# Kernel tuning notes

Measured on AMD Instinct MI355X. Metric: run time of the kernel, lower is better.

## Reference

```python
import jax, jax.numpy as jnp
import numpy as np
import math

DIM = 1024      # dim == dim_attn (required by value-reshape)
HEAD = 16
KV = 128        # K_v routing slots
HD = DIM // HEAD
N = 50000       # number of nodes


def setup_inputs() -> dict:
    key = jax.random.key(0)
    ks = jax.random.split(key, 8)
    s = lambda fan_in: 1.0 / np.sqrt(fan_in)
    return {
        "x": jax.random.normal(ks[0], (N, DIM), jnp.float32),
        "node_index": jax.random.normal(ks[1], (N, 4), jnp.float32),
        # nn.Linear(dim, dim_attn)
        "Wq": jax.random.normal(ks[2], (DIM, DIM), jnp.float32) * s(DIM),
        "bq": jnp.zeros((DIM,), jnp.float32),
        # nn.Parameter key (K_v, head, head_dim), torch.randn init
        "key_p": jax.random.normal(ks[3], (KV, HEAD, HD), jnp.float32),
        # nn.Linear(dim, dim)
        "Wv": jax.random.normal(ks[4], (DIM, DIM), jnp.float32) * s(DIM),
        "bv": jnp.zeros((DIM,), jnp.float32),
        # gate params, shape (head, 1)
        "alpha": jnp.full((HEAD, 1), math.log(9.0), jnp.float32),
        "beta": jnp.full((HEAD, 1), math.log(0.01), jnp.float32),
        # nn.Linear(4, head*K_v)
        "Wb": jax.random.normal(ks[5], (HEAD * KV, 4), jnp.float32) * s(4),
        "bb": jnp.zeros((HEAD * KV,), jnp.float32),
    }


def _mh_sinkhorn(A, num_iters=3, eps=0.05):
    # A: (N, H, K). Faithful to the per-head torch sinkhorn (Q transposed to
    # (K, N)): row sums are over the node axis, col sums over the slot axis.
    n = A.shape[0]
    k = A.shape[2]
    Q = jnp.exp(A / eps)
    Q = Q / jnp.sum(Q, axis=(0, 2), keepdims=True)          # total-sum norm per head
    for _ in range(num_iters):
        Q = Q / jnp.sum(Q, axis=0, keepdims=True) / k       # rows of Q.T (per slot)
        Q = Q / jnp.sum(Q, axis=2, keepdims=True) / n       # cols of Q.T (per node)
    return Q * n


def reference(x, node_index, Wq, bq, key_p, Wv, bv, alpha, beta, Wb, bb):
    n = x.shape[0]
    q = (x @ Wq.T + bq).reshape(n, HEAD, HD)
    attn = jnp.einsum('nhd,rhd->nhr', q, key_p) / np.float32(np.sqrt(HD))
    bias = (node_index @ Wb.T + bb).reshape(n, HEAD, KV)
    attn = attn + bias                                       # (n, H, K_v)
    xv = (x @ Wv.T + bv).reshape(n, HEAD, HD)
    v = jnp.einsum('nhr,nhd->rhd', jax.nn.sigmoid(attn), xv)  # (K_v, H, D)
    cons = _mh_sinkhorn(jax.nn.softmax(attn, axis=-1))
    v = jnp.einsum('nhr,rhd->nhd', cons, v)
    out = jax.nn.sigmoid(alpha) * xv + jax.nn.sigmoid(beta) * v  # (H,1) broadcasts
    return out.reshape(n, DIM)
```

## Files before the change

### kernel.cpp

```cpp
#include <hip/hip_runtime.h>

#define N_NODES 50000
#define MPAD    50176
#define DIM     1024
#define HEAD    16
#define KV      128
#define HD      64
#define NGRP    98

typedef unsigned short ushort_t;
typedef short short8 __attribute__((ext_vector_type(8)));
typedef float f32x4 __attribute__((ext_vector_type(4)));

__device__ inline unsigned short f2bf(float f){
  union { float f; unsigned u; } v; v.f = f;
  unsigned u = v.u;
  unsigned r = (u + 0x7FFFu + ((u >> 16) & 1u)) >> 16;
  return (unsigned short)r;
}
__device__ inline float bf2f(unsigned u16){
  union { unsigned u; float f; } v; v.u = (u16 & 0xFFFFu) << 16; return v.f;
}

__device__ inline void gload_lds16(const void* g, void* l){
  __builtin_amdgcn_global_load_lds(
      (const __attribute__((address_space(1))) void*)g,
      (__attribute__((address_space(3))) void*)l, 16, 0, 0);
}

__device__ inline short8 frag64(const ushort_t* lds, int row, int kk, int lane){
  int c  = kk*4 + (lane >> 4);
  int cc = c ^ (row & 7);
  return *(const short8*)(lds + row*64 + cc*8);
}
__device__ inline short8 frag128(const ushort_t* lds, int row, int kk, int lane){
  int c  = kk*4 + (lane >> 4);
  int cc = c ^ (row & 7);
  return *(const short8*)(lds + row*128 + cc*8);
}

__global__ void k_zero(float* p, int n){
  int i = blockIdx.x*256 + threadIdx.x;
  if (i < n) p[i] = 0.f;
}

__global__ void k_prep_x(const float* __restrict__ x, ushort_t* __restrict__ x_bf){
  int idx = blockIdx.x*256 + threadIdx.x;
  int row = idx >> 7, c = idx & 127;
  const float4* s = (const float4*)(x + (size_t)row*1024 + c*8);
  float4 f0 = s[0], f1 = s[1];
  short8 v;
  v[0]=(short)f2bf(f0.x); v[1]=(short)f2bf(f0.y); v[2]=(short)f2bf(f0.z); v[3]=(short)f2bf(f0.w);
  v[4]=(short)f2bf(f1.x); v[5]=(short)f2bf(f1.y); v[6]=(short)f2bf(f1.z); v[7]=(short)f2bf(f1.w);
  int sc = (c & ~7) | ((c ^ row) & 7);
  *(short8*)(x_bf + (size_t)row*1024 + sc*8) = v;
}

__global__ void k_prep_w(const float* __restrict__ Wq, const float* __restrict__ Wv,
                         ushort_t* __restrict__ w_bf){
  int idx = blockIdx.x*256 + threadIdx.x;
  int j = idx >> 10, k = idx & 1023;
  float v = (j < 1024) ? Wq[idx] : Wv[(size_t)(j-1024)*1024 + k];
  int d = k & 63;
  int scol = (k & ~63) | ((((d>>3) ^ (j & 7)) & 7) << 3) | (d & 7);
  w_bf[(size_t)j*1024 + scol] = f2bf(v);
}

__global__ void k_prep_key(const float* __restrict__ key_p, ushort_t* __restrict__ key_bf){
  int idx = blockIdx.x*256 + threadIdx.x;
  int h = idx >> 13, rem = idx & 8191;
  int r = rem >> 6, d = rem & 63;
  float v = key_p[(size_t)(r*HEAD + h)*HD + d];
  int pos = ((((d>>3) ^ (r & 7)) & 7) << 3) | (d & 7);
  key_bf[(size_t)h*8192 + r*64 + pos] = f2bf(v);
}

__global__ void k_vreduce(const float* __restrict__ vp, float* __restrict__ vout){
  int i = blockIdx.x*256 + threadIdx.x;
  float s = 0.f;
  for (int gg = 0; gg < NGRP; ++gg) s += vp[(size_t)gg*131072 + i];
  vout[i] = s;
}

__global__ __launch_bounds__(512) void k_gemm(const ushort_t* __restrict__ x_bf,
    const ushort_t* __restrict__ w_bf, const float* __restrict__ bq,
    const float* __restrict__ bv, ushort_t* __restrict__ q_bf, float* xv_out){
  extern __shared__ char gsm[];
  ushort_t* As = (ushort_t*)gsm;
  ushort_t* Bs = (ushort_t*)(gsm + 65536);
  const int tid = threadIdx.x, lane = tid & 63;
  const int wid = tid >> 6, wr = wid >> 2, wc = wid & 3;
  int b = blockIdx.x;
  int wg = (b & 7)*196 + (b >> 3);
  const int bm0 = (wg >> 3) * 256, bn0 = (wg & 7) * 256;

  f32x4 acc[8][4];
  #pragma unroll
  for (int m=0;m<8;m++)
    #pragma unroll
    for (int n=0;n<4;n++) acc[m][n] = (f32x4){0.f,0.f,0.f,0.f};

  const ushort_t* asrc = x_bf + (size_t)bm0*1024;
  const ushort_t* bsrc = w_bf + (size_t)bn0*1024;

#define STAGE(kt, bi)                                                    \
  { _Pragma("unroll")                                                    \
    for (int it=0; it<4; ++it){                                          \
      int chunk = it*512 + tid;                                          \
      int r = chunk >> 3, c = chunk & 7;                                 \
      gload_lds16(asrc + (size_t)r*1024 + (kt)*64 + c*8,                 \
                  As + (bi)*16384 + chunk*8);                            \
    }                                                                    \
    _Pragma("unroll")                                                    \
    for (int it=0; it<4; ++it){                                          \
      int chunk = it*512 + tid;                                          \
      int r = chunk >> 3, c = chunk & 7;                                 \
      gload_lds16(bsrc + (size_t)r*1024 + (kt)*64 + c*8,                 \
                  Bs + (bi)*16384 + chunk*8);                            \
    }                                                                    \
  }

  STAGE(0, 0);
  STAGE(1, 1);

  for (int kt = 0; kt < 16; ++kt){
    const int cur = kt & 1;
    if (kt == 15) { asm volatile("s_waitcnt vmcnt(0)" ::: "memory"); }
    else          { asm volatile("s_waitcnt vmcnt(8)" ::: "memory"); }
    __builtin_amdgcn_s_barrier();

    const ushort_t* ab  = As + cur*16384;
    const ushort_t* bb_ = Bs + cur*16384;
    #pragma unroll
    for (int kk=0;kk<2;kk++){
      short8 bfr[4];
      #pragma unroll
      for (int n=0;n<4;n++) bfr[n] = frag64(bb_, wc*64 + n*16 + (lane&15), kk, lane);
      #pragma unroll
      for (int m=0;m<8;m++){
        short8 af = frag64(ab, wr*128 + m*16 + (lane&15), kk, lane);
        #pragma unroll
        for (int n=0;n<4;n++)
          acc[m][n] = __builtin_amdgcn_mfma_f32_16x16x32_bf16(af, bfr[n], acc[m][n], 0,0,0);
      }
    }
    __builtin_amdgcn_s_barrier();
    if (kt + 2 < 16) STAGE(kt+2, cur);
  }
#undef STAGE

  __syncthreads();

  const bool isq = bn0 < 1024;
  float biasv[4];
  #pragma unroll
  for (int n=0;n<4;n++){
    int col = bn0 + wc*64 + n*16 + (lane & 15);
    biasv[n] = isq ? bq[col] : bv[col - 1024];
  }

  if (isq){
    ushort_t* img = (ushort_t*)gsm;
    #pragma unroll
    for (int n=0;n<4;n++){
      int lcol = wc*64 + n*16 + (lane & 15);
      int d = lcol & 63;
      #pragma unroll
      for (int m=0;m<8;m++){
        #pragma unroll
        for (int j=0;j<4;j++){
          int lrow = wr*128 + m*16 + (lane>>4)*4 + j;
          int sc = (lcol & ~63) | ((((d>>3) ^ (lrow & 7)) & 7) << 3) | (d & 7);
          img[lrow*256 + sc] = f2bf(acc[m][n][j] + biasv[n]);
        }
      }
    }
    __syncthreads();
    #pragma unroll
    for (int it=0; it<16; ++it){
      int r  = it*16 + (tid >> 5);
      int ch = tid & 31;
      short8 v = *(const short8*)(img + r*256 + ch*8);
      *(short8*)(q_bf + (size_t)(bm0 + r)*1024 + bn0 + ch*8) = v;
    }
  } else {
    #pragma unroll
    for (int n=0;n<4;n++){
      int col = bn0 + wc*64 + n*16 + (lane & 15);
      #pragma unroll
      for (int m=0;m<8;m++){
        #pragma unroll
        for (int j=0;j<4;j++){
          int row = bm0 + wr*128 + m*16 + (lane>>4)*4 + j;
          if (row < N_NODES)
            xv_out[(size_t)row*1024 + (col - 1024)] = acc[m][n][j] + biasv[n];
        }
      }
    }
  }
}

__global__ __launch_bounds__(256) void k_s1(const ushort_t* __restrict__ q_bf,
    const ushort_t* __restrict__ key_bf, const float* __restrict__ ni,
    const float* __restrict__ Wb, const float* __restrict__ bb,
    const float* __restrict__ cs_in, float* __restrict__ cs_out){
  __shared__ float col_acc[4][128];
  const int tid = threadIdx.x, lane = tid & 63, wid = tid >> 6;
  const int h   = blockIdx.x & 15;
  const int blk = blockIdx.x >> 4;
  const int gw  = blk*4 + wid;
  const int cl  = lane & 15, rg = lane >> 4;

  float wbv[8][4], bbr[8], wv[8];
  #pragma unroll
  for (int n=0;n<8;n++){
    int r = h*128 + n*16 + cl;
    float4 w4 = *(const float4*)(Wb + (size_t)r*4);
    wbv[n][0]=w4.x; wbv[n][1]=w4.y; wbv[n][2]=w4.z; wbv[n][3]=w4.w;
    bbr[n] = bb[r];
    wv[n]  = 1.f/(128.f*cs_in[r]);
  }
  short8 kf[8][2];
  #pragma unroll
  for (int n=0;n<8;n++)
    #pragma unroll
    for (int kk=0;kk<2;kk++){
      int c = (kk*4+rg) ^ (cl & 7);
      kf[n][kk] = *(const short8*)(key_bf + (size_t)h*8192 + (n*16+cl)*64 + c*8);
    }

  float cs_acc[8];
  #pragma unroll
  for (int n=0;n<8;n++) cs_acc[n] = 0.f;

  const int g0 = gw*8;
  short8 qc[2], qn[2];
  { int row = g0*16 + cl;
    #pragma unroll
    for (int kk=0;kk<2;kk++){
      int c = (kk*4+rg) ^ (row & 7);
      qc[kk] = *(const short8*)(q_bf + (size_t)row*1024 + h*64 + c*8);
    } }

  for (int u = 0; u < 8; ++u){
    const int i0 = (g0+u)*16;
    if (u+1 < 8){
      int row = i0 + 16 + cl;
      #pragma unroll
      for (int kk=0;kk<2;kk++){
        int c = (kk*4+rg) ^ (row & 7);
        qn[kk] = *(const short8*)(q_bf + (size_t)row*1024 + h*64 + c*8);
      }
    }
    float4 ni4[4];
    #pragma unroll
    for (int j=0;j<4;j++){
      int row = i0 + rg*4 + j;
      if (row < N_NODES) ni4[j] = *(const float4*)(ni + (size_t)row*4);
      else { ni4[j].x=0.f; ni4[j].y=0.f; ni4[j].z=0.f; ni4[j].w=0.f; }
    }
    f32x4 acc[8];
    #pragma unroll
    for (int n=0;n<8;n++) acc[n] = (f32x4){0.f,0.f,0.f,0.f};
    #pragma unroll
    for (int n=0;n<8;n++){
      acc[n] = __builtin_amdgcn_mfma_f32_16x16x32_bf16(qc[0], kf[n][0], acc[n], 0,0,0);
      acc[n] = __builtin_amdgcn_mfma_f32_16x16x32_bf16(qc[1], kf[n][1], acc[n], 0,0,0);
    }
    float a[8][4];
    #pragma unroll
    for (int n=0;n<8;n++)
      #pragma unroll
      for (int j=0;j<4;j++)
        a[n][j] = acc[n][j]*0.125f
                + wbv[n][0]*ni4[j].x + wbv[n][1]*ni4[j].y
                + wbv[n][2]*ni4[j].z + wbv[n][3]*ni4[j].w + bbr[n];

    float mj[4], sj[4];
    #pragma unroll
    for (int j=0;j<4;j++){
      float m0 = a[0][j];
      #pragma unroll
      for (int n=1;n<8;n++) m0 = fmaxf(m0, a[n][j]);
      m0 = fmaxf(m0, __shfl_xor(m0,1));
      m0 = fmaxf(m0, __shfl_xor(m0,2));
      m0 = fmaxf(m0, __shfl_xor(m0,4));
      m0 = fmaxf(m0, __shfl_xor(m0,8));
      mj[j] = m0;
    }
    #pragma unroll
    for (int j=0;j<4;j++){
      float s = 0.f;
      #pragma unroll
      for (int n=0;n<8;n++){ float e = __expf(a[n][j]-mj[j]); a[n][j]=e; s+=e; }
      s += __shfl_xor(s,1); s += __shfl_xor(s,2);
      s += __shfl_xor(s,4); s += __shfl_xor(s,8);
      sj[j] = s;
    }
    #pragma unroll
    for (int j=0;j<4;j++){
      float inv = 20.f/sj[j];
      #pragma unroll
      for (int n=0;n<8;n++) a[n][j] = __expf(a[n][j]*inv);
    }
    float uj[4];
    #pragma unroll
    for (int j=0;j<4;j++){
      float s = 0.f;
      #pragma unroll
      for (int n=0;n<8;n++) s += a[n][j]*wv[n];
      s += __shfl_xor(s,1); s += __shfl_xor(s,2);
      s += __shfl_xor(s,4); s += __shfl_xor(s,8);
      int row = i0 + rg*4 + j;
      uj[j] = (row < N_NODES) ? 1.f/(50000.f*s) : 0.f;
    }
    #pragma unroll
    for (int n=0;n<8;n++)
      cs_acc[n] += a[n][0]*uj[0] + a[n][1]*uj[1] + a[n][2]*uj[2] + a[n][3]*uj[3];

    qc[0] = qn[0]; qc[1] = qn[1];
  }

  #pragma unroll
  for (int n=0;n<8;n++){
    float v = cs_acc[n];
    v += __shfl_xor(v,16); v += __shfl_xor(v,32);
    cs_acc[n] = v;
  }
  if (rg == 0){
    #pragma unroll
    for (int n=0;n<8;n++) col_acc[wid][n*16+cl] = cs_acc[n];
  }
  __syncthreads();
  if (tid < 128)
    atomicAdd(&cs_out[h*128+tid],
      col_acc[0][tid]+col_acc[1][tid]+col_acc[2][tid]+col_acc[3][tid]);
}

__global__ __launch_bounds__(256) void k_s2(const ushort_t* __restrict__ q_bf,
    const ushort_t* __restrict__ key_bf, const float* __restrict__ ni,
    const float* __restrict__ Wb, const float* __restrict__ bb,
    const float* __restrict__ cs_in, const float* __restrict__ v_fin,
    float* xv_out, const float* __restrict__ alpha, const float* __restrict__ beta){
  __shared__ ushort_t key_lds[128*64];
  __shared__ ushort_t vT[64*128];
  __shared__ ushort_t consW[4][16*128];
  const int tid = threadIdx.x, lane = tid & 63, wid = tid >> 6;
  const int h   = blockIdx.x & 15;
  const int blk = blockIdx.x >> 4;
  const int gw  = blk*4 + wid;
  const int cl  = lane & 15, rg = lane >> 4;

  #pragma unroll
  for (int it = 0; it < 4; ++it){
    int chunk = it*256 + tid;
    gload_lds16(key_bf + (size_t)h*8192 + chunk*8, key_lds + chunk*8);
  }
  { int r = tid >> 1, dh = (tid & 1)*32;
    #pragma unroll
    for (int i=0;i<32;i++){
      int d = dh + i;
      vT[d*128 + ((r>>3) ^ (d&7))*8 + (r&7)] = f2bf(v_fin[((size_t)r*16 + h)*64 + d]);
    } }

  float wbv[8][4], bbr[8], wv[8];
  #pragma unroll
  for (int n=0;n<8;n++){
    int r = h*128 + n*16 + cl;
    float4 w4 = *(const float4*)(Wb + (size_t)r*4);
    wbv[n][0]=w4.x; wbv[n][1]=w4.y; wbv[n][2]=w4.z; wbv[n][3]=w4.w;
    bbr[n] = bb[r];
    wv[n]  = 1.f/(128.f*cs_in[r]);
  }
  const float sa = 1.f/(1.f + __expf(-alpha[h]));
  const float sb = 1.f/(1.f + __expf(-beta[h]));

  __syncthreads();

  ushort_t* cw = consW[wid];
  const int g0 = gw*8;
  short8 qc[2], qn[2];
  { int row = g0*16 + cl;
    #pragma unroll
    for (int kk=0;kk<2;kk++){
      int c = (kk*4+rg) ^ (row & 7);
      qc[kk] = *(const short8*)(q_bf + (size_t)row*1024 + h*64 + c*8);
    } }

  for (int u = 0; u < 8; ++u){
    const int i0 = (g0+u)*16;
    if (u+1 < 8){
      int row = i0 + 16 + cl;
      #pragma unroll
      for (int kk=0;kk<2;kk++){
        int c = (kk*4+rg) ^ (row & 7);
        qn[kk] = *(const short8*)(q_bf + (size_t)row*1024 + h*64 + c*8);
      }
    }
    float4 ni4[4];
    #pragma unroll
    for (int j=0;j<4;j++){
      int row = i0 + rg*4 + j;
      if (row < N_NODES) ni4[j] = *(const float4*)(ni + (size_t)row*4);
      else { ni4[j].x=0.f; ni4[j].y=0.f; ni4[j].z=0.f; ni4[j].w=0.f; }
    }
    f32x4 acc[8];
    #pragma unroll
    for (int n=0;n<8;n++) acc[n] = (f32x4){0.f,0.f,0.f,0.f};
    #pragma unroll
    for (int n=0;n<8;n++){
      short8 k0 = frag64(key_lds, n*16+cl, 0, lane);
      short8 k1 = frag64(key_lds, n*16+cl, 1, lane);
      acc[n] = __builtin_amdgcn_mfma_f32_16x16x32_bf16(qc[0], k0, acc[n], 0,0,0);
      acc[n] = __builtin_amdgcn_mfma_f32_16x16x32_bf16(qc[1], k1, acc[n], 0,0,0);
    }
    float a[8][4];
    #pragma unroll
    for (int n=0;n<8;n++)
      #pragma unroll
      for (int j=0;j<4;j++)
        a[n][j] = acc[n][j]*0.125f
                + wbv[n][0]*ni4[j].x + wbv[n][1]*ni4[j].y
                + wbv[n][2]*ni4[j].z + wbv[n][3]*ni4[j].w + bbr[n];

    float mj[4], sj[4];
    #pragma unroll
    for (int j=0;j<4;j++){
      float m0 = a[0][j];
      #pragma unroll
      for (int n=1;n<8;n++) m0 = fmaxf(m0, a[n][j]);
      m0 = fmaxf(m0, __shfl_xor(m0,1));
      m0 = fmaxf(m0, __shfl_xor(m0,2));
      m0 = fmaxf(m0, __shfl_xor(m0,4));
      m0 = fmaxf(m0, __shfl_xor(m0,8));
      mj[j] = m0;
    }
    #pragma unroll
    for (int j=0;j<4;j++){
      float s = 0.f;
      #pragma unroll
      for (int n=0;n<8;n++){ float e = __expf(a[n][j]-mj[j]); a[n][j]=e; s+=e; }
      s += __shfl_xor(s,1); s += __shfl_xor(s,2);
      s += __shfl_xor(s,4); s += __shfl_xor(s,8);
      sj[j] = s;
    }
    #pragma unroll
    for (int j=0;j<4;j++){
      float inv = 20.f/sj[j];
      #pragma unroll
      for (int n=0;n<8;n++) a[n][j] = __expf(a[n][j]*inv);
    }
    float scj[4];
    #pragma unroll
    for (int j=0;j<4;j++){
      float s = 0.f;
      #pragma unroll
      for (int n=0;n<8;n++) s += a[n][j]*wv[n];
      s += __shfl_xor(s,1); s += __shfl_xor(s,2);
      s += __shfl_xor(s,4); s += __shfl_xor(s,8);
      scj[j] = 1.f/s;
    }
    #pragma unroll
    for (int n=0;n<8;n++){
      #pragma unroll
      for (int j=0;j<4;j++){
        int node = rg*4 + j;
        int r = n*16 + cl;
        int ch = (r>>3) ^ (node & 7);
        cw[node*128 + ch*8 + (r&7)] = f2bf(scj[j]*a[n][j]*wv[n]);
      }
    }
    f32x4 oac[4];
    #pragma unroll
    for (int nf=0;nf<4;nf++) oac[nf] = (f32x4){0.f,0.f,0.f,0.f};
    #pragma unroll
    for (int ks=0; ks<4; ++ks){
      short8 ca = frag128(cw, cl, ks, lane);
      #pragma unroll
      for (int nf=0;nf<4;nf++){
        short8 vb = frag128(vT, nf*16+cl, ks, lane);
        oac[nf] = __builtin_amdgcn_mfma_f32_16x16x32_bf16(ca, vb, oac[nf], 0,0,0);
      }
    }
    #pragma unroll
    for (int j=0;j<4;j++){
      int row = i0 + rg*4 + j;
      if (row < N_NODES){
        #pragma unroll
        for (int nf=0;nf<4;nf++){
          size_t ad = (size_t)row*1024 + h*64 + nf*16 + cl;
          xv_out[ad] = sa*xv_out[ad] + sb*oac[nf][j];
        }
      }
    }
    qc[0] = qn[0]; qc[1] = qn[1];
  }
}

template<int PHASE>
__global__ __launch_bounds__(256) void k_attn(
    const ushort_t* __restrict__ q_bf, const ushort_t* __restrict__ key_bf,
    const float* __restrict__ node_index, const float* __restrict__ Wb,
    const float* __restrict__ bb, const float* __restrict__ colsum_in,
    float* __restrict__ colsum_out, const float* __restrict__ v_fin,
    float* __restrict__ v_part, float* xv_out,
    const float* __restrict__ alpha, const float* __restrict__ beta)
{
  constexpr int QB    = 2;
  constexpr int O_Q   = 0;
  constexpr int O_KEY = O_Q + QB*8192;
  constexpr int O_NI  = O_KEY + 16384;
  constexpr int O_WB  = O_NI + QB*1024;
  constexpr int O_RED = O_WB + 2560;
  constexpr int O_COL = O_RED + 2048;
  constexpr int O_W   = O_COL + 512;
  constexpr int O_X1  = O_W + 512;
  constexpr int O_X2  = O_X1 + 16384;

  extern __shared__ char smem[];
  ushort_t* q_lds   = (ushort_t*)(smem + O_Q);
  ushort_t* key_lds = (ushort_t*)(smem + O_KEY);
  float* ni_lds  = (float*)(smem + O_NI);
  float* wb_lds  = (float*)(smem + O_WB);
  float* red_lds = (float*)(smem + O_RED);
  float* col_acc = (float*)(smem + O_COL);
  ushort_t* sigT = (ushort_t*)(smem + O_X1);
  ushort_t* xvT  = (ushort_t*)(smem + O_X2);

  const int tid = threadIdx.x, lane = tid & 63, wid = tid >> 6;
  const int h    = blockIdx.x & 15;
  const int g    = blockIdx.x >> 4;
  const int base = g * 512;
  int NT = (MPAD - base) >> 6; if (NT > 8) NT = 8;

  #pragma unroll
  for (int it = 0; it < 4; ++it){
    int chunk = it*256 + tid;
    gload_lds16(key_bf + (size_t)h*8192 + chunk*8, key_lds + chunk*8);
  }
  #pragma unroll
  for (int it = 0; it < 2; ++it){
    int chunk = it*256 + tid;
    int r = chunk >> 3, c = chunk & 7;
    gload_lds16(q_bf + (size_t)(base + r)*1024 + h*64 + c*8, q_lds + chunk*8);
  }
  { int r = tid >> 2, c = tid & 3;
    ni_lds[tid] = (base + r < N_NODES) ? node_index[(size_t)(base + r)*4 + c] : 0.f; }
  if (tid < 128){
    #pragma unroll
    for (int c=0;c<4;c++) wb_lds[tid*5+c] = Wb[(size_t)(h*128 + tid)*4 + c];
    wb_lds[tid*5+4] = bb[h*128 + tid];
    col_acc[tid] = 0.f;
  }
  float xvr[16], xvn[16];
  { int d = tid & 63, q4 = tid >> 6;
    #pragma unroll
    for (int i=0;i<16;i++){
      int row = base + q4*16 + i;
      xvr[i] = (row < N_NODES) ? xv_out[(size_t)row*1024 + h*64 + d] : 0.f;
    } }
  f32x4 vac[2][4];
  for (int m=0;m<2;m++) for (int n=0;n<4;n++) vac[m][n] = (f32x4){0.f,0.f,0.f,0.f};

  __syncthreads();

  for (int t = 0; t < NT; ++t){
    const int i0  = base + t*64;
    const int cur = t & 1;
    const ushort_t* qb  = q_lds  + cur*4096;
    const float*    nib = ni_lds + cur*256;
    float ni_next = 0.f;

    if (t+1 < NT){
      int i1 = i0 + 64;
      #pragma unroll
      for (int it = 0; it < 2; ++it){
        int chunk = it*256 + tid;
        int r = chunk >> 3, c = chunk & 7;
        gload_lds16(q_bf + (size_t)(i1 + r)*1024 + h*64 + c*8,
                    q_lds + (cur^1)*4096 + chunk*8);
      }
      int r = tid >> 2, c = tid & 3;
      ni_next = (i0 + 64 + r < N_NODES) ? node_index[(size_t)(i0+64+r)*4 + c] : 0.f;
      int d = tid & 63, q4 = tid >> 6;
      #pragma unroll
      for (int i=0;i<16;i++){
        int row = i0 + 64 + q4*16 + i;
        xvn[i] = (row < N_NODES) ? xv_out[(size_t)row*1024 + h*64 + d] : 0.f;
      }
    }

    f32x4 acc[2][4];
    for (int m=0;m<2;m++) for (int n=0;n<4;n++) acc[m][n] = (f32x4){0.f,0.f,0.f,0.f};
    #pragma unroll
    for (int kk = 0; kk < 2; ++kk){
      short8 kf[2];
      #pragma unroll
      for (int m=0;m<2;m++) kf[m] = frag64(key_lds, wid*32 + m*16 + (lane&15), kk, lane);
      #pragma unroll
      for (int n=0;n<4;n++){
        short8 qf = frag64(qb, n*16 + (lane&15), kk, lane);
        #pragma unroll
        for (int m=0;m<2;m++)
          acc[m][n] = __builtin_amdgcn_mfma_f32_16x16x32_bf16(kf[m], qf, acc[m][n], 0,0,0);
      }
    }

    float nif[4][4];
    #pragma unroll
    for (int n=0;n<4;n++){
      int nn = n*16 + (lane&15);
      #pragma unroll
      for (int c=0;c<4;c++) nif[n][c] = nib[nn*4+c];
    }
    float a[2][4][4];
    #pragma unroll
    for (int m=0;m<2;m++){
      #pragma unroll
      for (int j=0;j<4;j++){
        int r = wid*32 + m*16 + (lane>>4)*4 + j;
        float w0 = wb_lds[r*5+0], w1 = wb_lds[r*5+1];
        float w2 = wb_lds[r*5+2], w3 = wb_lds[r*5+3], w4 = wb_lds[r*5+4];
        #pragma unroll
        for (int n=0;n<4;n++){
          float b = w4 + w0*nif[n][0] + w1*nif[n][1] + w2*nif[n][2] + w3*nif[n][3];
          a[m][n][j] = acc[m][n][j]*0.125f + b;
        }
      }
    }

    float vmask[4];
    #pragma unroll
    for (int n=0;n<4;n++) vmask[n] = (i0 + n*16 + (lane&15) < N_NODES) ? 1.f : 0.f;

    #pragma unroll
    for (int m=0;m<2;m++) for (int n=0;n<4;n++) for (int j=0;j<4;j++){
      int r  = wid*32 + m*16 + (lane>>4)*4 + j;
      int nn = n*16 + (lane&15);
      float sg = vmask[n] / (1.f + __expf(-a[m][n][j]));
      sigT[r*64 + ((((nn>>3) ^ (r&7)) & 7) << 3) + (nn&7)] = f2bf(sg);
    }
    { int d = tid & 63, q4 = tid >> 6;
      #pragma unroll
      for (int i=0;i<16;i++){
        int nn = q4*16 + i;
        xvT[d*64 + ((((nn>>3) ^ (d&7)) & 7) << 3) + (nn&7)] = f2bf(xvr[i]);
      }
    }

    float pm[4];
    #pragma unroll
    for (int n=0;n<4;n++){
      float m0 = a[0][n][0];
      #pragma unroll
      for (int m=0;m<2;m++) for (int j=0;j<4;j++) m0 = fmaxf(m0, a[m][n][j]);
      m0 = fmaxf(m0, __shfl_xor(m0, 16));
      m0 = fmaxf(m0, __shfl_xor(m0, 32));
      pm[n] = m0;
    }
    if (lane < 16){
      #pragma unroll
      for (int n=0;n<4;n++) red_lds[wid*64 + n*16 + lane] = pm[n];
    }
    __syncthreads();

    float mnn[4], snn[4];
    #pragma unroll
    for (int n=0;n<4;n++){
      int nn = n*16 + (lane&15);
      float m0 = red_lds[nn];
      m0 = fmaxf(m0, red_lds[64+nn]); m0 = fmaxf(m0, red_lds[128+nn]); m0 = fmaxf(m0, red_lds[192+nn]);
      mnn[n] = m0;
    }
    #pragma unroll
    for (int n=0;n<4;n++){
      float s = 0.f;
      #pragma unroll
      for (int m=0;m<2;m++) for (int j=0;j<4;j++){
        float e = __expf(a[m][n][j] - mnn[n]);
        a[m][n][j] = e; s += e;
      }
      s += __shfl_xor(s, 16); s += __shfl_xor(s, 32);
      snn[n] = s;
    }
    if (lane < 16){
      #pragma unroll
      for (int n=0;n<4;n++) red_lds[256 + wid*64 + n*16 + lane] = snn[n];
    }

    #pragma unroll
    for (int kk=0;kk<2;kk++){
      short8 sa[2];
      #pragma unroll
      for (int m=0;m<2;m++) sa[m] = frag64(sigT, wid*32 + m*16 + (lane&15), kk, lane);
      #pragma unroll
      for (int n=0;n<4;n++){
        short8 xf = frag64(xvT, n*16 + (lane&15), kk, lane);
        #pragma unroll
        for (int m=0;m<2;m++)
          vac[m][n] = __builtin_amdgcn_mfma_f32_16x16x32_bf16(sa[m], xf, vac[m][n], 0,0,0);
      }
    }
    __syncthreads();

    #pragma unroll
    for (int n=0;n<4;n++){
      int nn = n*16 + (lane&15);
      snn[n] = red_lds[256+nn] + red_lds[256+64+nn] + red_lds[256+128+nn] + red_lds[256+192+nn];
    }
    #pragma unroll
    for (int n=0;n<4;n++){
      float inv = 20.f / snn[n];
      #pragma unroll
      for (int m=0;m<2;m++) for (int j=0;j<4;j++)
        a[m][n][j] = __expf(a[m][n][j] * inv);
    }

    float cs[2][4];
    #pragma unroll
    for (int m=0;m<2;m++){
      #pragma unroll
      for (int j=0;j<4;j++){
        float s = 0.f;
        #pragma unroll
        for (int n=0;n<4;n++) s += a[m][n][j] * vmask[n];
        s += __shfl_xor(s, 1); s += __shfl_xor(s, 2);
        s += __shfl_xor(s, 4); s += __shfl_xor(s, 8);
        cs[m][j] = s;
      }
    }
    if ((lane & 15) == 0){
      #pragma unroll
      for (int m=0;m<2;m++) for (int j=0;j<4;j++){
        int r = wid*32 + m*16 + (lane>>4)*4 + j;
        col_acc[r] += cs[m][j];
      }
    }

    if (t+1 < NT){
      ni_lds[(cur^1)*256 + tid] = ni_next;
      #pragma unroll
      for (int i=0;i<16;i++) xvr[i] = xvn[i];
    }
    __syncthreads();
  }

  { float* vdst = v_part + (size_t)g*131072;
    #pragma unroll
    for (int m=0;m<2;m++) for (int n=0;n<4;n++) for (int j=0;j<4;j++){
      int r = wid*32 + m*16 + (lane>>4)*4 + j;
      int d = n*16 + (lane&15);
      vdst[((size_t)r*16 + h)*64 + d] = vac[m][n][j];
    } }
  if (tid < 128) atomicAdd(&colsum_out[h*128 + tid], col_acc[tid]);
}

extern "C" void kernel_launch(void* const* d_in, const int* in_sizes, int n_in,
                              void* d_out, int out_size, void* d_ws, size_t ws_size,
                              hipStream_t stream){
  const float* x     = (const float*)d_in[0];
  const float* ni    = (const float*)d_in[1];
  const float* Wq    = (const float*)d_in[2];
  const float* bq    = (const float*)d_in[3];
  const float* keyp  = (const float*)d_in[4];
  const float* Wv    = (const float*)d_in[5];
  const float* bv    = (const float*)d_in[6];
  const float* alpha = (const float*)d_in[7];
  const float* beta  = (const float*)d_in[8];
  const float* Wb    = (const float*)d_in[9];
  const float* bb    = (const float*)d_in[10];
  float* out = (float*)d_out;

  char* ws = (char*)d_ws;
  ushort_t* x_bf   = (ushort_t*)(ws);
  float*    v_part = (float*)(ws);
  ushort_t* q_bf   = (ushort_t*)(ws + 102760448);
  ushort_t* w_bf   = (ushort_t*)(ws + 205520896);
  ushort_t* key_bf = (ushort_t*)(ws + 209715200);
  float*    v_fin  = (float*)(ws + 209977344);
  float*    cs     = (float*)(ws + 210501632);

  (void)hipFuncSetAttribute((const void*)k_gemm,
      hipFuncAttributeMaxDynamicSharedMemorySize, 131072);

  k_zero<<<dim3(24), 256, 0, stream>>>(cs, 6144);
  k_zero<<<dim3(704), 256, 0, stream>>>((float*)(x_bf + (size_t)N_NODES*1024), 90112);
  k_prep_x<<<dim3(25000), 256, 0, stream>>>(x, x_bf);
  k_prep_w<<<dim3(2048*1024/256), 256, 0, stream>>>(Wq, Wv, w_bf);
  k_prep_key<<<dim3(HEAD*KV*HD/256), 256, 0, stream>>>(keyp, key_bf);
  k_gemm<<<dim3(1568), 512, 131072, stream>>>(x_bf, w_bf, bq, bv, q_bf, out);

  dim3 ag(NGRP*16);
  k_attn<0><<<ag, 256, 65024, stream>>>(q_bf, key_bf, ni, Wb, bb, nullptr, cs, v_fin, v_part, out, alpha, beta);
  k_vreduce<<<dim3(512), 256, 0, stream>>>(v_part, v_fin);
  k_s1<<<dim3(1568), 256, 0, stream>>>(q_bf, key_bf, ni, Wb, bb, cs,      cs+2048);
  k_s1<<<dim3(1568), 256, 0, stream>>>(q_bf, key_bf, ni, Wb, bb, cs+2048, cs+4096);
  k_s2<<<dim3(1568), 256, 0, stream>>>(q_bf, key_bf, ni, Wb, bb, cs+4096, v_fin, out, alpha, beta);
}
```

Before: 934.8 us.

## Split QV GEMM into two launches, stage keys in LDS, halve s1/s2 work per wave

The fused Q/V GEMM launch is split into two templated launches, one producing Q and one producing V, each with 784 blocks. This removes the runtime isq branch and lets each variant be specialised. In k_s1, the per-wave register-resident key fragments are replaced by a shared LDS copy loaded once per block, which cuts register pressure. k_s1 and k_s2 now process 4 node groups per wave instead of 8 with twice as many blocks, raising parallelism at the cost of more per-block setup (Wb and key loads).

```diff
diff --git a/kernel.cpp b/kernel.cpp
--- a/kernel.cpp
+++ b/kernel.cpp
@@ -82,6 +82,7 @@
   vout[i] = s;
 }
 
+template<int HALF>
 __global__ __launch_bounds__(512) void k_gemm(const ushort_t* __restrict__ x_bf,
     const ushort_t* __restrict__ w_bf, const float* __restrict__ bq,
     const float* __restrict__ bv, ushort_t* __restrict__ q_bf, float* xv_out){
@@ -91,8 +92,9 @@
   const int tid = threadIdx.x, lane = tid & 63;
   const int wid = tid >> 6, wr = wid >> 2, wc = wid & 3;
   int b = blockIdx.x;
-  int wg = (b & 7)*196 + (b >> 3);
-  const int bm0 = (wg >> 3) * 256, bn0 = (wg & 7) * 256;
+  int wg = (b & 7)*98 + (b >> 3);
+  const int bm0 = (wg >> 2) * 256;
+  const int bn0 = HALF*1024 + (wg & 3) * 256;
 
   f32x4 acc[8][4];
   #pragma unroll
@@ -151,15 +153,14 @@
 
   __syncthreads();
 
-  const bool isq = bn0 < 1024;
   float biasv[4];
   #pragma unroll
   for (int n=0;n<4;n++){
     int col = bn0 + wc*64 + n*16 + (lane & 15);
-    biasv[n] = isq ? bq[col] : bv[col - 1024];
-  }
-
-  if (isq){
+    biasv[n] = (HALF == 0) ? bq[col] : bv[col - 1024];
+  }
+
+  if (HALF == 0){
     ushort_t* img = (ushort_t*)gsm;
     #pragma unroll
     for (int n=0;n<4;n++){
@@ -204,6 +205,7 @@
     const ushort_t* __restrict__ key_bf, const float* __restrict__ ni,
     const float* __restrict__ Wb, const float* __restrict__ bb,
     const float* __restrict__ cs_in, float* __restrict__ cs_out){
+  __shared__ ushort_t key_lds[128*64];
   __shared__ float col_acc[4][128];
   const int tid = threadIdx.x, lane = tid & 63, wid = tid >> 6;
   const int h   = blockIdx.x & 15;
@@ -211,6 +213,12 @@
   const int gw  = blk*4 + wid;
   const int cl  = lane & 15, rg = lane >> 4;
 
+  #pragma unroll
+  for (int it = 0; it < 4; ++it){
+    int chunk = it*256 + tid;
+    gload_lds16(key_bf + (size_t)h*8192 + chunk*8, key_lds + chunk*8);
+  }
+
   float wbv[8][4], bbr[8], wv[8];
   #pragma unroll
   for (int n=0;n<8;n++){
@@ -220,20 +228,13 @@
     bbr[n] = bb[r];
     wv[n]  = 1.f/(128.f*cs_in[r]);
   }
-  short8 kf[8][2];
-  #pragma unroll
-  for (int n=0;n<8;n++)
-    #pragma unroll
-    for (int kk=0;kk<2;kk++){
-      int c = (kk*4+rg) ^ (cl & 7);
-      kf[n][kk] = *(const short8*)(key_bf + (size_t)h*8192 + (n*16+cl)*64 + c*8);
-    }
-
   float cs_acc[8];
   #pragma unroll
   for (int n=0;n<8;n++) cs_acc[n] = 0.f;
 
-  const int g0 = gw*8;
+  __syncthreads();
+
+  const int g0 = gw*4;
   short8 qc[2], qn[2];
   { int row = g0*16 + cl;
     #pragma unroll
@@ -242,9 +243,9 @@
       qc[kk] = *(const short8*)(q_bf + (size_t)row*1024 + h*64 + c*8);
     } }
 
-  for (int u = 0; u < 8; ++u){
+  for (int u = 0; u < 4; ++u){
     const int i0 = (g0+u)*16;
-    if (u+1 < 8){
+    if (u+1 < 4){
       int row = i0 + 16 + cl;
       #pragma unroll
       for (int kk=0;kk<2;kk++){
@@ -264,8 +265,10 @@
     for (int n=0;n<8;n++) acc[n] = (f32x4){0.f,0.f,0.f,0.f};
     #pragma unroll
     for (int n=0;n<8;n++){
-      acc[n] = __builtin_amdgcn_mfma_f32_16x16x32_bf16(qc[0], kf[n][0], acc[n], 0,0,0);
-      acc[n] = __builtin_amdgcn_mfma_f32_16x16x32_bf16(qc[1], kf[n][1], acc[n], 0,0,0);
+      short8 k0 = frag64(key_lds, n*16+cl, 0, lane);
+      short8 k1 = frag64(key_lds, n*16+cl, 1, lane);
+      acc[n] = __builtin_amdgcn_mfma_f32_16x16x32_bf16(qc[0], k0, acc[n], 0,0,0);
+      acc[n] = __builtin_amdgcn_mfma_f32_16x16x32_bf16(qc[1], k1, acc[n], 0,0,0);
     }
     float a[8][4];
     #pragma unroll
@@ -378,7 +381,7 @@
   __syncthreads();
 
   ushort_t* cw = consW[wid];
-  const int g0 = gw*8;
+  const int g0 = gw*4;
   short8 qc[2], qn[2];
   { int row = g0*16 + cl;
     #pragma unroll
@@ -387,9 +390,9 @@
       qc[kk] = *(const short8*)(q_bf + (size_t)row*1024 + h*64 + c*8);
     } }
 
-  for (int u = 0; u < 8; ++u){
+  for (int u = 0; u < 4; ++u){
     const int i0 = (g0+u)*16;
-    if (u+1 < 8){
+    if (u+1 < 4){
       int row = i0 + 16 + cl;
       #pragma unroll
       for (int kk=0;kk<2;kk++){
@@ -780,7 +783,9 @@
   float*    v_fin  = (float*)(ws + 209977344);
   float*    cs     = (float*)(ws + 210501632);
 
-  (void)hipFuncSetAttribute((const void*)k_gemm,
+  (void)hipFuncSetAttribute((const void*)k_gemm<0>,
+      hipFuncAttributeMaxDynamicSharedMemorySize, 131072);
+  (void)hipFuncSetAttribute((const void*)k_gemm<1>,
       hipFuncAttributeMaxDynamicSharedMemorySize, 131072);
 
   k_zero<<<dim3(24), 256, 0, stream>>>(cs, 6144);
@@ -788,12 +793,13 @@
   k_prep_x<<<dim3(25000), 256, 0, stream>>>(x, x_bf);
   k_prep_w<<<dim3(2048*1024/256), 256, 0, stream>>>(Wq, Wv, w_bf);
   k_prep_key<<<dim3(HEAD*KV*HD/256), 256, 0, stream>>>(keyp, key_bf);
-  k_gemm<<<dim3(1568), 512, 131072, stream>>>(x_bf, w_bf, bq, bv, q_bf, out);
+  k_gemm<0><<<dim3(784), 512, 131072, stream>>>(x_bf, w_bf, bq, bv, q_bf, out);
+  k_gemm<1><<<dim3(784), 512, 131072, stream>>>(x_bf, w_bf, bq, bv, q_bf, out);
 
   dim3 ag(NGRP*16);
   k_attn<0><<<ag, 256, 65024, stream>>>(q_bf, key_bf, ni, Wb, bb, nullptr, cs, v_fin, v_part, out, alpha, beta);
   k_vreduce<<<dim3(512), 256, 0, stream>>>(v_part, v_fin);
-  k_s1<<<dim3(1568), 256, 0, stream>>>(q_bf, key_bf, ni, Wb, bb, cs,      cs+2048);
-  k_s1<<<dim3(1568), 256, 0, stream>>>(q_bf, key_bf, ni, Wb, bb, cs+2048, cs+4096);
-  k_s2<<<dim3(1568), 256, 0, stream>>>(q_bf, key_bf, ni, Wb, bb, cs+4096, v_fin, out, alpha, beta);
-}
+  k_s1<<<dim3(3136), 256, 0, stream>>>(q_bf, key_bf, ni, Wb, bb, cs,      cs+2048);
+  k_s1<<<dim3(3136), 256, 0, stream>>>(q_bf, key_bf, ni, Wb, bb, cs+2048, cs+4096);
+  k_s2<<<dim3(3136), 256, 0, stream>>>(q_bf, key_bf, ni, Wb, bb, cs+4096, v_fin, out, alpha, beta);
+}
```

After: 935.4 us. No clear change (+0.1%).
